# Performance work log

Hardware: AMD Instinct MI355X
Metric: run time of the kernel (lower is better)

The kernel has to match this reference:

```python
import jax, jax.numpy as jnp
from jax import lax
import numpy as np

B, NR, NC, FEAT = 8, 1024, 1024, 768
N = NR + NC
HID, GATD, GRUD = 256, 128, 64
NEG = -9e15  # matches -9000000000000000.0 in torch source


def setup_inputs() -> dict:
    key = jax.random.key(0)
    ks = jax.random.split(key, 24)
    s = 0.02
    nrm = lambda k, shp: jax.random.normal(k, shp, jnp.float32) * s
    z = lambda shp: jnp.zeros(shp, jnp.float32)
    inp = {}
    inp['req_nodes'] = jax.random.normal(ks[0], (B, NR, FEAT), jnp.float32)
    inp['code_nodes'] = jax.random.normal(ks[1], (B, NC, FEAT), jnp.float32)
    inp['alignment_matrix'] = jax.random.bernoulli(ks[2], 0.05, (B, N, N)).astype(jnp.float32)
    inp['total_nodes'] = jax.random.randint(ks[3], (B,), N // 2, N + 1).astype(jnp.int32)
    # feature_projection
    inp['W_proj'] = nrm(ks[4], (HID, FEAT)); inp['b_proj'] = z((HID,))
    # GAT layer 1 (HID->HID), attention weight a is Linear(2*HID, 1, bias=False)
    inp['W_g1'] = nrm(ks[5], (HID, HID)); inp['b_g1'] = z((HID,)); inp['a_g1'] = nrm(ks[6], (2 * HID,))
    # GAT layer 2 (HID->GATD)
    inp['W_g2'] = nrm(ks[7], (GATD, HID)); inp['b_g2'] = z((GATD,)); inp['a_g2'] = nrm(ks[8], (2 * GATD,))
    # bidirectional GRU (torch layout: [3H, in], gates r|z|n)
    inp['Wih_f'] = nrm(ks[9], (3 * GRUD, GATD)); inp['Whh_f'] = nrm(ks[10], (3 * GRUD, GRUD))
    inp['bih_f'] = z((3 * GRUD,)); inp['bhh_f'] = z((3 * GRUD,))
    inp['Wih_b'] = nrm(ks[11], (3 * GRUD, GATD)); inp['Whh_b'] = nrm(ks[12], (3 * GRUD, GRUD))
    inp['bih_b'] = z((3 * GRUD,)); inp['bhh_b'] = z((3 * GRUD,))
    inp['W_fus'] = nrm(ks[13], (GRUD, 2 * GRUD)); inp['b_fus'] = z((GRUD,))
    inp['W_c1'] = nrm(ks[14], (HID // 2, GRUD)); inp['b_c1'] = z((HID // 2,))
    inp['W_c2'] = nrm(ks[15], (1, HID // 2)); inp['b_c2'] = z((1,))
    return inp


def _gat_layer(x, adj, mask, W, b, a):
    # h: [B, N, D]
    h = x @ W.T + b
    D = h.shape[-1]
    # attention(concat(h_i, h_j)) == a[:D]@h_i + a[D:]@h_j -> never materialize [B,N,N,2D]
    s_src = h @ a[:D]   # [B, N]
    s_dst = h @ a[D:]   # [B, N]
    e = jax.nn.leaky_relu(s_src[:, :, None] + s_dst[:, None, :], 0.01)  # [B,N,N]
    att = jax.nn.softmax(jnp.where(adj > 0, e, NEG), axis=-1)
    out = jnp.einsum('bij,bjd->bid', att, h)
    return out * mask[..., None]


def _gru_dir(xproj, Whh, bhh, reverse):
    # xproj: [B, T, 3H] = x @ Wih.T + bih (precomputed)
    Bv, H = xproj.shape[0], Whh.shape[1]
    def step(h, xt):
        gh = h @ Whh.T + bhh
        ir, iz, inn = jnp.split(xt, 3, axis=-1)
        hr, hz, hn = jnp.split(gh, 3, axis=-1)
        r = jax.nn.sigmoid(ir + hr)
        zt = jax.nn.sigmoid(iz + hz)
        n = jnp.tanh(inn + r * hn)
        hnew = (1.0 - zt) * n + zt * h
        return hnew, hnew
    h0 = jnp.zeros((Bv, H), xproj.dtype)
    _, ys = lax.scan(step, h0, jnp.swapaxes(xproj, 0, 1), reverse=reverse)
    return jnp.swapaxes(ys, 0, 1)  # [B, T, H]


def _forward(req_nodes, code_nodes, alignment_matrix, total_nodes,
             W_proj, b_proj, W_g1, b_g1, a_g1, W_g2, b_g2, a_g2,
             Wih_f, Whh_f, bih_f, bhh_f, Wih_b, Whh_b, bih_b, bhh_b,
             W_fus, b_fus, W_c1, b_c1, W_c2, b_c2):
    x = jnp.concatenate([req_nodes, code_nodes], axis=1)        # [B, N, FEAT]
    proj = jax.nn.relu(x @ W_proj.T + b_proj)                   # dropout is eval-mode identity
    Nt = proj.shape[1]
    mask = (jnp.arange(Nt)[None, :] < total_nodes[:, None]).astype(proj.dtype)  # [B, N]
    g1 = _gat_layer(proj, alignment_matrix, mask, W_g1, b_g1, a_g1)
    g1 = jax.nn.relu(g1) * mask[..., None]
    gat_out = _gat_layer(g1, alignment_matrix, mask, W_g2, b_g2, a_g2)
    gat_out = gat_out * mask[..., None]  # extra masking as in torch source (idempotent)
    gf = _gru_dir(gat_out @ Wih_f.T + bih_f, Whh_f, bhh_f, reverse=False)
    gb = _gru_dir(gat_out @ Wih_b.T + bih_b, Whh_b, bhh_b, reverse=True)
    gru_out = jnp.concatenate([gf, gb], axis=-1) * mask[..., None]  # [B, N, 2*GRUD]
    fused = gru_out @ W_fus.T + b_fus                               # [B, N, GRUD]
    pooled = jnp.mean(fused, axis=1)  # AdaptiveAvgPool1d(1) over seq dim
    h1 = jax.nn.relu(pooled @ W_c1.T + b_c1)
    out = jax.nn.sigmoid(h1 @ W_c2.T + b_c2)  # [B, 1]
    return out


def reference(req_nodes, code_nodes, alignment_matrix, total_nodes,
              W_proj, b_proj, W_g1, b_g1, a_g1, W_g2, b_g2, a_g2,
              Wih_f, Whh_f, bih_f, bhh_f, Wih_b, Whh_b, bih_b, bhh_b,
              W_fus, b_fus, W_c1, b_c1, W_c2, b_c2):
    return _forward(req_nodes, code_nodes, alignment_matrix, total_nodes,
                    W_proj, b_proj, W_g1, b_g1, a_g1, W_g2, b_g2, a_g2,
                    Wih_f, Whh_f, bih_f, bhh_f, Wih_b, Whh_b, bih_b, bhh_b,
                    W_fus, b_fus, W_c1, b_c1, W_c2, b_c2)
```

## Files before the change

### kernel.cpp

```cpp
#include <hip/hip_runtime.h>
#include <stdint.h>

#define EMAX 256

typedef short bf16x8 __attribute__((ext_vector_type(8)));
typedef float f32x4 __attribute__((ext_vector_type(4)));
typedef _Float16 h2_t __attribute__((ext_vector_type(2)));

#define SWZ(r, c) ((r) * 64 + ((c) ^ (((r) & 7) << 3)))
#define SWZ256(r, c) ((r) * 256 + ((c) ^ (((r) & 7) << 3)))

__device__ __forceinline__ uint16_t f2bf(float f) {
    union { float f; uint32_t u; } v; v.f = f;
    uint32_t u = v.u;
    uint32_t r = (u + 0x7FFFu + ((u >> 16) & 1u)) >> 16;
    return (uint16_t)r;
}
__device__ __forceinline__ float bf2f(uint16_t h) {
    union { uint32_t u; float f; } v; v.u = ((uint32_t)h) << 16;
    return v.f;
}
__device__ __forceinline__ h2_t u2h2(uint32_t u) {
    union { uint32_t u; h2_t h; } v; v.u = u;
    return v.h;
}
__device__ __forceinline__ uint32_t cvtpk_bf16(float lo, float hi) {
    uint32_t d;
    asm("v_cvt_pk_bf16_f32 %0, %1, %2" : "=v"(d) : "v"(lo), "v"(hi));
    return d;
}

__global__ __launch_bounds__(256) void k_prep(const float* wp, const float* wg1, const float* wg2,
                                              const float* wif, const float* wib,
                                              const float* whf, const float* whb,
                                              const float* bihf, const float* bihb,
                                              uint16_t* op, uint16_t* og1, uint16_t* og2,
                                              uint16_t* oifb, _Float16* ohf, _Float16* ohb, float* bihfb,
                                              float* __restrict__ Sz) {
    int i = blockIdx.x * 256 + threadIdx.x;
    if (i < 196608) op[i]  = f2bf(wp[i]);
    if (i < 65536)  og1[i] = f2bf(wg1[i]);
    if (i < 32768)  og2[i] = f2bf(wg2[i]);
    if (i < 24576)  { oifb[i] = f2bf(wif[i]); oifb[24576 + i] = f2bf(wib[i]); }
    if (i < 12288)  { ohf[i] = (_Float16)whf[i]; ohb[i] = (_Float16)whb[i]; }
    if (i < 192)    { bihfb[i] = bihf[i]; bihfb[192 + i] = bihb[i]; }
    if (i < 1024)   Sz[i] = 0.f;
}

__global__ __launch_bounds__(256) void k_edge(const float* __restrict__ adj,
                                              uint16_t* __restrict__ eidx, int* __restrict__ ecnt) {
    int wid  = threadIdx.x >> 6, lane = threadIdx.x & 63;
    int gw   = blockIdx.x * 4 + wid;
    const float4* base = (const float4*)adj + lane;
    float4 va[8], vb[8];
#define LOADROW(dst, r) { const float4* p_ = base + (size_t)(r) * 512; \
        _Pragma("unroll") for (int c_ = 0; c_ < 8; ++c_) dst[c_] = p_[c_ * 64]; }
#define PROCROW(src, r) { \
        uint32_t m4[8]; int c4[8]; \
        _Pragma("unroll") for (int c_ = 0; c_ < 8; ++c_) { \
            uint32_t m_ = (src[c_].x > 0.f ? 1u : 0u) | (src[c_].y > 0.f ? 2u : 0u) \
                        | (src[c_].z > 0.f ? 4u : 0u) | (src[c_].w > 0.f ? 8u : 0u); \
            m4[c_] = m_; c4[c_] = __popc(m_); } \
        int pk[4]; \
        _Pragma("unroll") for (int q_ = 0; q_ < 4; ++q_) pk[q_] = c4[2*q_] | (c4[2*q_+1] << 16); \
        _Pragma("unroll") for (int off_ = 1; off_ < 64; off_ <<= 1) { \
            _Pragma("unroll") for (int q_ = 0; q_ < 4; ++q_) { \
                int o_ = __shfl_up(pk[q_], off_); \
                if (lane >= off_) pk[q_] += o_; } } \
        uint16_t* outr = eidx + (size_t)(r) * EMAX; \
        int bse = 0; \
        _Pragma("unroll") for (int c_ = 0; c_ < 8; ++c_) { \
            int incl = (pk[c_ >> 1] >> ((c_ & 1) * 16)) & 0xffff; \
            int Tc_  = __shfl(incl, 63); \
            int p_   = bse + incl - c4[c_]; \
            uint32_t mm = m4[c_]; \
            int cb = c_ * 256 + lane * 4; \
            while (mm) { int k_ = __builtin_ctz(mm); mm &= mm - 1u; \
                if (p_ < EMAX) outr[p_] = (uint16_t)(cb + k_); ++p_; } \
            bse += Tc_; } \
        if (lane == 0) ecnt[r] = (bse < EMAX) ? bse : EMAX; }

    LOADROW(va, gw)
#pragma unroll
    for (int it = 0; it < 4; ++it) {
        int rA = gw + (2 * it) * 2048;
        int rB = rA + 2048;
        LOADROW(vb, rB)
        PROCROW(va, rA)
        if (it < 3) LOADROW(va, rB + 2048)
        PROCROW(vb, rB)
    }
#undef LOADROW
#undef PROCROW
}

__global__ __launch_bounds__(256) void k_l1(const float* __restrict__ req, const float* __restrict__ code,
                                            const uint16_t* __restrict__ Wp, const float* __restrict__ bp,
                                            const uint16_t* __restrict__ Wg1, const float* __restrict__ bg1,
                                            const float* __restrict__ a1,
                                            uint16_t* __restrict__ H1,
                                            float* __restrict__ s1src, float* __restrict__ s1dst) {
    __shared__ __align__(16) uint16_t As[64 * 64];
    __shared__ __align__(16) uint16_t Bs[4][64 * 64];
    __shared__ __align__(16) uint16_t Ps[64 * 256];
    int tid = threadIdx.x;
    int m0 = blockIdx.x * 64;
    int wave = tid >> 6, lane = tid & 63;
    int quad = lane >> 4, l16 = lane & 15;
    int ar = tid >> 3, ac = (tid & 7) * 8;
    f32x4 acc[16] = {};
    const float4* rowp[2];
#pragma unroll
    for (int h = 0; h < 2; ++h) {
        int n = m0 + ar + h * 32;
        int b = n >> 11, n2 = n & 2047;
        const float* s = (n2 < 1024) ? (req  + ((size_t)(b * 1024 + n2)) * 768)
                                     : (code + ((size_t)(b * 1024 + (n2 - 1024))) * 768);
        rowp[h] = (const float4*)s + (ac >> 2);
    }
    for (int kb = 0; kb < 768; kb += 64) {
#pragma unroll
        for (int h = 0; h < 2; ++h) {
            float4 f0 = rowp[h][(kb >> 2) + 0];
            float4 f1 = rowp[h][(kb >> 2) + 1];
            uint4 pk;
            pk.x = cvtpk_bf16(f0.x, f0.y); pk.y = cvtpk_bf16(f0.z, f0.w);
            pk.z = cvtpk_bf16(f1.x, f1.y); pk.w = cvtpk_bf16(f1.z, f1.w);
            *(uint4*)&As[SWZ(ar + h * 32, ac)] = pk;
        }
#pragma unroll
        for (int h = 0; h < 8; ++h) {
            int grow = ar + h * 32;
            *(uint4*)&Bs[grow >> 6][SWZ(grow & 63, ac)] =
                *(const uint4*)(Wp + (size_t)grow * 768 + kb + ac);
        }
        __syncthreads();
#pragma unroll
        for (int kk = 0; kk < 64; kk += 32) {
            bf16x8 af = *(bf16x8*)&As[SWZ(wave * 16 + l16, kk + quad * 8)];
#pragma unroll
            for (int c = 0; c < 16; ++c) {
                bf16x8 bfr = *(bf16x8*)&Bs[c >> 2][SWZ((c & 3) * 16 + l16, kk + quad * 8)];
                acc[c] = __builtin_amdgcn_mfma_f32_16x16x32_bf16(af, bfr, acc[c], 0, 0, 0);
            }
        }
        __syncthreads();
    }
#pragma unroll
    for (int c = 0; c < 16; ++c) {
        int col = c * 16 + l16;
        float bv = bp[col];
#pragma unroll
        for (int rg = 0; rg < 4; ++rg) {
            int row = wave * 16 + quad * 4 + rg;
            float v = fmaxf(acc[c][rg] + bv, 0.f);
            Ps[row * 256 + (col ^ ((row & 7) << 3))] = f2bf(v);
            acc[c][rg] = 0.f;
        }
    }
    __syncthreads();
    for (int kb = 0; kb < 256; kb += 64) {
#pragma unroll
        for (int h = 0; h < 8; ++h) {
            int grow = ar + h * 32;
            *(uint4*)&Bs[grow >> 6][SWZ(grow & 63, ac)] =
                *(const uint4*)(Wg1 + (size_t)grow * 256 + kb + ac);
        }
        __syncthreads();
#pragma unroll
        for (int kk = 0; kk < 64; kk += 32) {
            int row = wave * 16 + l16;
            int kcol = kb + kk + quad * 8;
            bf16x8 af = *(bf16x8*)&Ps[row * 256 + (kcol ^ ((row & 7) << 3))];
#pragma unroll
            for (int c = 0; c < 16; ++c) {
                bf16x8 bfr = *(bf16x8*)&Bs[c >> 2][SWZ((c & 3) * 16 + l16, kk + quad * 8)];
                acc[c] = __builtin_amdgcn_mfma_f32_16x16x32_bf16(af, bfr, acc[c], 0, 0, 0);
            }
        }
        __syncthreads();
    }
    float sA[4] = {0.f, 0.f, 0.f, 0.f}, sB[4] = {0.f, 0.f, 0.f, 0.f};
#pragma unroll
    for (int c = 0; c < 16; ++c) {
        int col = c * 16 + l16;
        float bv = bg1[col];
        float av1 = a1[col], av2 = a1[256 + col];
#pragma unroll
        for (int rg = 0; rg < 4; ++rg) {
            int row = m0 + wave * 16 + quad * 4 + rg;
            uint16_t hb = f2bf(acc[c][rg] + bv);
            H1[(size_t)row * 256 + col] = hb;
            float vr = bf2f(hb);
            sA[rg] = fmaf(vr, av1, sA[rg]);
            sB[rg] = fmaf(vr, av2, sB[rg]);
        }
    }
#pragma unroll
    for (int off = 1; off < 16; off <<= 1) {
#pragma unroll
        for (int rg = 0; rg < 4; ++rg) {
            sA[rg] += __shfl_xor(sA[rg], off);
            sB[rg] += __shfl_xor(sB[rg], off);
        }
    }
    if (l16 == 0) {
#pragma unroll
        for (int rg = 0; rg < 4; ++rg) {
            int row = m0 + wave * 16 + quad * 4 + rg;
            s1src[row] = sA[rg];
            s1dst[row] = sB[rg];
        }
    }
}

__global__ __launch_bounds__(256) void k_l2(const uint16_t* __restrict__ G1,
                                            const uint16_t* __restrict__ Wg2,
                                            const float* __restrict__ bg2,
                                            const float* __restrict__ a2,
                                            uint16_t* __restrict__ H2,
                                            float* __restrict__ s2src, float* __restrict__ s2dst) {
    __shared__ __align__(16) uint16_t As[64 * 64];
    __shared__ __align__(16) uint16_t Bs[2][64 * 64];
    int tid = threadIdx.x;
    int m0 = blockIdx.x * 64;
    int wave = tid >> 6, lane = tid & 63;
    int quad = lane >> 4, l16 = lane & 15;
    int ar = tid >> 3, ac = (tid & 7) * 8;
    f32x4 acc[8] = {};
    for (int kb = 0; kb < 256; kb += 64) {
        *(uint4*)&As[SWZ(ar, ac)]      = *(const uint4*)(G1 + (size_t)(m0 + ar)      * 256 + kb + ac);
        *(uint4*)&As[SWZ(ar + 32, ac)] = *(const uint4*)(G1 + (size_t)(m0 + ar + 32) * 256 + kb + ac);
#pragma unroll
        for (int h = 0; h < 4; ++h) {
            int grow = ar + h * 32;
            *(uint4*)&Bs[grow >> 6][SWZ(grow & 63, ac)] =
                *(const uint4*)(Wg2 + (size_t)grow * 256 + kb + ac);
        }
        __syncthreads();
#pragma unroll
        for (int kk = 0; kk < 64; kk += 32) {
            bf16x8 af = *(bf16x8*)&As[SWZ(wave * 16 + l16, kk + quad * 8)];
#pragma unroll
            for (int c = 0; c < 8; ++c) {
                bf16x8 bfr = *(bf16x8*)&Bs[c >> 2][SWZ((c & 3) * 16 + l16, kk + quad * 8)];
                acc[c] = __builtin_amdgcn_mfma_f32_16x16x32_bf16(af, bfr, acc[c], 0, 0, 0);
            }
        }
        __syncthreads();
    }
    float sA[4] = {0.f, 0.f, 0.f, 0.f}, sB[4] = {0.f, 0.f, 0.f, 0.f};
#pragma unroll
    for (int c = 0; c < 8; ++c) {
        int col = c * 16 + l16;
        float bv = bg2[col];
        float av1 = a2[col], av2 = a2[128 + col];
#pragma unroll
        for (int rg = 0; rg < 4; ++rg) {
            int row = m0 + wave * 16 + quad * 4 + rg;
            uint16_t hb = f2bf(acc[c][rg] + bv);
            H2[(size_t)row * 128 + col] = hb;
            float vr = bf2f(hb);
            sA[rg] = fmaf(vr, av1, sA[rg]);
            sB[rg] = fmaf(vr, av2, sB[rg]);
        }
    }
#pragma unroll
    for (int off = 1; off < 16; off <<= 1) {
#pragma unroll
        for (int rg = 0; rg < 4; ++rg) {
            sA[rg] += __shfl_xor(sA[rg], off);
            sB[rg] += __shfl_xor(sB[rg], off);
        }
    }
    if (l16 == 0) {
#pragma unroll
        for (int rg = 0; rg < 4; ++rg) {
            int row = m0 + wave * 16 + quad * 4 + rg;
            s2src[row] = sA[rg];
            s2dst[row] = sB[rg];
        }
    }
}

template<int ACT, int MODE>
__global__ __launch_bounds__(256) void k_gemm(const uint16_t* __restrict__ A,
                                              const uint16_t* __restrict__ Bw,
                                              const float* __restrict__ bias,
                                              void* __restrict__ Cv, void* __restrict__ Cv2,
                                              int M, int N, int K) {
    __shared__ __align__(16) uint16_t As[64 * 64];
    __shared__ __align__(16) uint16_t Bs[64 * 64];
    int tid = threadIdx.x;
    int n0 = blockIdx.x * 64, m0 = blockIdx.y * 64;
    int wave = tid >> 6, lane = tid & 63;
    int quad = lane >> 4, l16 = lane & 15;
    f32x4 acc[4] = {};
    int ar = tid >> 3;
    int ac = (tid & 7) * 8;
    for (int kb = 0; kb < K; kb += 64) {
        *(uint4*)&As[SWZ(ar, ac)]      = *(const uint4*)(A  + (size_t)(m0 + ar)      * K + kb + ac);
        *(uint4*)&As[SWZ(ar + 32, ac)] = *(const uint4*)(A  + (size_t)(m0 + ar + 32) * K + kb + ac);
        *(uint4*)&Bs[SWZ(ar, ac)]      = *(const uint4*)(Bw + (size_t)(n0 + ar)      * K + kb + ac);
        *(uint4*)&Bs[SWZ(ar + 32, ac)] = *(const uint4*)(Bw + (size_t)(n0 + ar + 32) * K + kb + ac);
        __syncthreads();
#pragma unroll
        for (int kk = 0; kk < 64; kk += 32) {
            bf16x8 af = *(bf16x8*)&As[SWZ(wave * 16 + l16, kk + quad * 8)];
#pragma unroll
            for (int c = 0; c < 4; ++c) {
                bf16x8 bfr = *(bf16x8*)&Bs[SWZ(c * 16 + l16, kk + quad * 8)];
                acc[c] = __builtin_amdgcn_mfma_f32_16x16x32_bf16(af, bfr, acc[c], 0, 0, 0);
            }
        }
        __syncthreads();
    }
#pragma unroll
    for (int c = 0; c < 4; ++c) {
        int col = n0 + c * 16 + l16;
        float bv = bias ? bias[col] : 0.f;
#pragma unroll
        for (int rg = 0; rg < 4; ++rg) {
            int row = m0 + wave * 16 + quad * 4 + rg;
            float v = acc[c][rg] + bv;
            if (ACT == 1) v = fmaxf(v, 0.f);
            if (MODE == 1)      ((uint16_t*)Cv)[(size_t)row * N + col] = f2bf(v);
            else if (MODE == 0) ((float*)Cv)[(size_t)row * N + col] = v;
            else {
                int tc = (col < 192) ? col : col - 192;
                int dc = (tc & 63) * 4 + (tc >> 6);
                float* dst = (col < 192) ? (float*)Cv : (float*)Cv2;
                dst[(size_t)row * 256 + dc] = v;
            }
        }
    }
}

#define ACC4(hv, wv) { \
    a0 = fmaf(wv, bf2f((uint16_t)(hv).x), a0); \
    a1 = fmaf(wv, bf2f((uint16_t)((hv).x >> 16)), a1); \
    a2 = fmaf(wv, bf2f((uint16_t)(hv).y), a2); \
    a3 = fmaf(wv, bf2f((uint16_t)((hv).y >> 16)), a3); }

template<int D, int LAYER1>
__global__ __launch_bounds__(256) void k_agg(const uint16_t* __restrict__ H,
                                             const float* __restrict__ ssrc,
                                             const float* __restrict__ sdst,
                                             const uint16_t* __restrict__ eidx,
                                             const int* __restrict__ ecnt,
                                             const int* __restrict__ total,
                                             uint16_t* __restrict__ out) {
    constexpr int LPG = (D == 256) ? 64 : 32;
    constexpr int G   = 64 / LPG;
    constexpr int RS  = D / 4;
    __shared__ __align__(16) uint2 ew[4][EMAX];
    int tid  = threadIdx.x;
    int wid  = tid >> 6, lane = tid & 63;
    int grp  = lane / LPG;
    int c    = lane % LPG;
    int b    = blockIdx.x & 7;
    int i    = ((blockIdx.x >> 3) << 2) + wid;
    int row  = (b << 11) + i;
    uint2* orow = (uint2*)(out + (size_t)row * D);
    if (i >= total[b]) {
        if (grp == 0) { uint2 z; z.x = 0u; z.y = 0u; orow[c] = z; }
        return;
    }
    int cnt = ecnt[row];
    const uint2* H2 = (const uint2*)(H + (size_t)b * 2048 * D);
    float a0 = 0.f, a1 = 0.f, a2 = 0.f, a3 = 0.f;
    if (cnt > 0) {
        float sv = ssrc[row];
        const uint16_t* er = eidx + (size_t)row * EMAX;
        int   jj[4]; float ee[4];
#pragma unroll
        for (int k = 0; k < 4; ++k) {
            int t = lane + 64 * k;
            int j = (t < cnt) ? (int)er[t] : 0;
            float x = sv + sdst[b * 2048 + j];
            float e = (x > 0.f) ? x : 0.01f * x;
            if (t >= cnt) e = -1e30f;
            jj[k] = j; ee[k] = e;
        }
        float m = fmaxf(fmaxf(ee[0], ee[1]), fmaxf(ee[2], ee[3]));
#pragma unroll
        for (int off = 32; off; off >>= 1) m = fmaxf(m, __shfl_xor(m, off));
        float w[4]; float s = 0.f;
#pragma unroll
        for (int k = 0; k < 4; ++k) { w[k] = __expf(ee[k] - m); s += w[k]; }
#pragma unroll
        for (int off = 32; off; off >>= 1) s += __shfl_xor(s, off);
        float inv = 1.f / s;
#pragma unroll
        for (int k = 0; k < 4; ++k) {
            uint2 p; p.x = (uint32_t)jj[k]; p.y = __float_as_uint(w[k] * inv);
            ew[wid][lane + 64 * k] = p;
        }
        asm volatile("s_waitcnt lgkmcnt(0)" ::: "memory");
        constexpr int EPB = 4 * G;
        int cntP = (cnt + EPB - 1) & ~(EPB - 1);
        if constexpr (G == 1) {
            for (int t = 0; t < cntP; t += 4) {
                uint2 e0 = ew[wid][t + 0], e1 = ew[wid][t + 1];
                uint2 e2 = ew[wid][t + 2], e3 = ew[wid][t + 3];
                uint2 h0 = H2[(size_t)e0.x * RS + c];
                uint2 h1 = H2[(size_t)e1.x * RS + c];
                uint2 h2 = H2[(size_t)e2.x * RS + c];
                uint2 h3 = H2[(size_t)e3.x * RS + c];
                ACC4(h0, __uint_as_float(e0.y));
                ACC4(h1, __uint_as_float(e1.y));
                ACC4(h2, __uint_as_float(e2.y));
                ACC4(h3, __uint_as_float(e3.y));
            }
        } else {
            for (int t = 0; t < cntP; t += 8) {
                uint2 e0 = ew[wid][t + 0 + grp], e1 = ew[wid][t + 2 + grp];
                uint2 e2 = ew[wid][t + 4 + grp], e3 = ew[wid][t + 6 + grp];
                uint2 h0 = H2[(size_t)e0.x * RS + c];
                uint2 h1 = H2[(size_t)e1.x * RS + c];
                uint2 h2 = H2[(size_t)e2.x * RS + c];
                uint2 h3 = H2[(size_t)e3.x * RS + c];
                ACC4(h0, __uint_as_float(e0.y));
                ACC4(h1, __uint_as_float(e1.y));
                ACC4(h2, __uint_as_float(e2.y));
                ACC4(h3, __uint_as_float(e3.y));
            }
        }
    } else {
        for (int t = grp; t < 2048; t += G) {
            uint2 hv = H2[(size_t)t * RS + c];
            ACC4(hv, 1.f);
        }
        a0 *= (1.f / 2048.f); a1 *= (1.f / 2048.f);
        a2 *= (1.f / 2048.f); a3 *= (1.f / 2048.f);
    }
    if constexpr (G == 2) {
        a0 += __shfl_xor(a0, 32); a1 += __shfl_xor(a1, 32);
        a2 += __shfl_xor(a2, 32); a3 += __shfl_xor(a3, 32);
    }
    if (LAYER1) {
        a0 = fmaxf(a0, 0.f); a1 = fmaxf(a1, 0.f);
        a2 = fmaxf(a2, 0.f); a3 = fmaxf(a3, 0.f);
    }
    if (grp == 0) {
        uint2 pk;
        pk.x = (uint32_t)f2bf(a0) | ((uint32_t)f2bf(a1) << 16);
        pk.y = (uint32_t)f2bf(a2) | ((uint32_t)f2bf(a3) << 16);
        orow[c] = pk;
    }
}

#define CHUNKS 16
#define CLEN   128
#define WARM   64
#define FDOT2(acc, p, wq) acc = __builtin_amdgcn_fdot2(p, u2h2(wq), acc, false)
#define DOTBLK(hq, q) { \
    h2_t p0 = u2h2(hq.x), p1 = u2h2(hq.y), p2 = u2h2(hq.z), p3 = u2h2(hq.w); \
    FDOT2(ar0, p0, wr[4*q+0]); FDOT2(ar1, p1, wr[4*q+1]); FDOT2(ar2, p2, wr[4*q+2]); FDOT2(ar3, p3, wr[4*q+3]); \
    FDOT2(az0, p0, wz[4*q+0]); FDOT2(az1, p1, wz[4*q+1]); FDOT2(az2, p2, wz[4*q+2]); FDOT2(az3, p3, wz[4*q+3]); \
    FDOT2(an0, p0, wn[4*q+0]); FDOT2(an1, p1, wn[4*q+1]); FDOT2(an2, p2, wn[4*q+2]); FDOT2(an3, p3, wn[4*q+3]); }
#define GRU_STEP(xq) { \
    uint4 h0 = hv4[0], h1 = hv4[1], h2v = hv4[2], h3 = hv4[3]; \
    uint4 h4 = hv4[4], h5 = hv4[5], h6 = hv4[6], h7 = hv4[7]; \
    float ar0 = br, ar1 = 0.f, ar2 = 0.f, ar3 = 0.f; \
    float az0 = bz, az1 = 0.f, az2 = 0.f, az3 = 0.f; \
    float an0 = bn, an1 = 0.f, an2 = 0.f, an3 = 0.f; \
    DOTBLK(h0, 0) DOTBLK(h1, 1) DOTBLK(h2v, 2) DOTBLK(h3, 3) \
    DOTBLK(h4, 4) DOTBLK(h5, 5) DOTBLK(h6, 6) DOTBLK(h7, 7) \
    float ghr = (ar0 + ar1) + (ar2 + ar3); \
    float ghz = (az0 + az1) + (az2 + az3); \
    float ghn = (an0 + an1) + (an2 + an3); \
    float er = __expf(-(xq.x + ghr)); \
    float r = __builtin_amdgcn_rcpf(1.f + er); \
    float ez = __expf(-(xq.y + ghz)); \
    float z = __builtin_amdgcn_rcpf(1.f + ez); \
    float nv = fmaf(r, ghn, xq.z); \
    float en = __expf(-2.f * nv); \
    float n = fmaf(-2.f, __builtin_amdgcn_rcpf(1.f + en), 1.f); \
    hj = fmaf(z, hj - n, n); \
    sj += (t < Tcur) ? hj : 0.f; \
    hb[j] = (_Float16)hj; \
    asm volatile("" ::: "memory"); \
    t += dt; }

__global__ __attribute__((amdgpu_flat_work_group_size(64, 64), amdgpu_waves_per_eu(1, 1)))
void k_gru(const float* __restrict__ XPf, const float* __restrict__ XPb,
           const _Float16* __restrict__ WhF, const _Float16* __restrict__ WhB,
           const float* __restrict__ bhh_f, const float* __restrict__ bhh_b,
           const int* __restrict__ total,
           float* __restrict__ S) {
    int blk   = blockIdx.x;
    int chunk = blk & (CHUNKS - 1);
    int sc    = blk >> 4;
    int dir   = sc >> 3;
    int b     = sc & 7;
    int j     = threadIdx.x;
    const float* XP  = dir ? XPb : XPf;
    const uint32_t* Wd = (const uint32_t*)(dir ? WhB : WhF);
    const float* bhh = dir ? bhh_b : bhh_f;
    uint32_t wr[32], wz[32], wn[32];
#pragma unroll
    for (int c = 0; c < 32; ++c) {
        wr[c] = Wd[(size_t)(      j) * 32 + c];
        wz[c] = Wd[(size_t)( 64 + j) * 32 + c];
        wn[c] = Wd[(size_t)(128 + j) * 32 + c];
    }
    float br = bhh[j], bz = bhh[64 + j], bn = bhh[128 + j];
    __shared__ __align__(16) _Float16 hbuf[64];
    _Float16* hb = hbuf;
    hb[j] = (_Float16)0.f;
    asm volatile("s_waitcnt lgkmcnt(0)" ::: "memory");
    float hj = 0.f, sj = 0.f;
    int Tb = total[b];
    int s0 = chunk * CLEN - WARM;
    int W0 = WARM;
    if (s0 < 0) { s0 = 0; W0 = 0; }
    const float4* xbase = (const float4*)(XP + (size_t)b * 2048 * 256) + j;
    int xstep = dir ? -64 : 64;
    const float4* xptr = xbase + (size_t)(dir ? (2047 - s0) : s0) * 64;
    float4 x0 = *xptr; xptr += xstep;
    float4 x1 = *xptr; xptr += xstep;
    float4 x2 = *xptr; xptr += xstep;
    float4 x3 = *xptr; xptr += xstep;
    int t = dir ? (2047 - s0) : s0, dt = dir ? -1 : 1;
    const uint4* hv4 = (const uint4*)hb;
    int Tcur = -1;
    for (int su = 0; su < W0; su += 4) {
        GRU_STEP(x0) x0 = *xptr; xptr += xstep;
        GRU_STEP(x1) x1 = *xptr; xptr += xstep;
        GRU_STEP(x2) x2 = *xptr; xptr += xstep;
        GRU_STEP(x3) x3 = *xptr; xptr += xstep;
    }
    Tcur = Tb;
    for (int su = 0; su < CLEN; su += 4) {
        GRU_STEP(x0) x0 = *xptr; xptr += xstep;
        GRU_STEP(x1) x1 = *xptr; xptr += xstep;
        GRU_STEP(x2) x2 = *xptr; xptr += xstep;
        GRU_STEP(x3) x3 = *xptr; xptr += xstep;
    }
    atomicAdd(&S[b * 128 + dir * 64 + j], sj);
}

__global__ __launch_bounds__(128) void k_final(const float* __restrict__ S,
                                               const float* __restrict__ Wfus, const float* __restrict__ bfus,
                                               const float* __restrict__ Wc1, const float* __restrict__ bc1,
                                               const float* __restrict__ Wc2, const float* __restrict__ bc2,
                                               float* __restrict__ out) {
    __shared__ float pool[64];
    __shared__ float red[128];
    int tid = threadIdx.x;
    for (int b = 0; b < 8; ++b) {
        if (tid < 64) {
            float a = 0.f;
            for (int jj = 0; jj < 128; ++jj) a += S[b * 128 + jj] * Wfus[tid * 128 + jj];
            pool[tid] = bfus[tid] + a * (1.f / 2048.f);
        }
        __syncthreads();
        float a1 = 0.f;
        for (int d = 0; d < 64; ++d) a1 += pool[d] * Wc1[tid * 64 + d];
        float h = fmaxf(a1 + bc1[tid], 0.f);
        red[tid] = h * Wc2[tid];
        __syncthreads();
        for (int s = 64; s; s >>= 1) { if (tid < s) red[tid] += red[tid + s]; __syncthreads(); }
        if (tid == 0) out[b] = 1.f / (1.f + __expf(-(red[0] + bc2[0])));
        __syncthreads();
    }
}

extern "C" void kernel_launch(void* const* d_in, const int* in_sizes, int n_in,
                              void* d_out, int out_size, void* d_ws, size_t ws_size,
                              hipStream_t stream) {
    (void)in_sizes; (void)n_in; (void)out_size; (void)ws_size;
    const float* req   = (const float*)d_in[0];
    const float* code  = (const float*)d_in[1];
    const float* adj   = (const float*)d_in[2];
    const int*   total = (const int*)  d_in[3];
    const float* W_proj = (const float*)d_in[4];
    const float* b_proj = (const float*)d_in[5];
    const float* W_g1   = (const float*)d_in[6];
    const float* b_g1   = (const float*)d_in[7];
    const float* a_g1   = (const float*)d_in[8];
    const float* W_g2   = (const float*)d_in[9];
    const float* b_g2   = (const float*)d_in[10];
    const float* a_g2   = (const float*)d_in[11];
    const float* Wih_f  = (const float*)d_in[12];
    const float* Whh_f  = (const float*)d_in[13];
    const float* bih_f  = (const float*)d_in[14];
    const float* bhh_f  = (const float*)d_in[15];
    const float* Wih_b  = (const float*)d_in[16];
    const float* Whh_b  = (const float*)d_in[17];
    const float* bih_b  = (const float*)d_in[18];
    const float* bhh_b  = (const float*)d_in[19];
    const float* W_fus  = (const float*)d_in[20];
    const float* b_fus  = (const float*)d_in[21];
    const float* W_c1   = (const float*)d_in[22];
    const float* b_c1   = (const float*)d_in[23];
    const float* W_c2   = (const float*)d_in[24];
    const float* b_c2   = (const float*)d_in[25];

    char* ws = (char*)d_ws;
    float*    XPf  = (float*)(ws + 4096);
    float*    XPb  = (float*)(ws + 4096 + 16777216 + 4096);
    uint16_t* EIDX = (uint16_t*)(ws + 25169920);
    uint16_t* WPb  = (uint16_t*)(ws + 33570816);
    uint16_t* WG1b = (uint16_t*)(ws + 33964032);
    uint16_t* WG2b = (uint16_t*)(ws + 34095104);
    uint16_t* WIFB = (uint16_t*)(ws + 34160640);
    uint16_t* H1bf = (uint16_t*)(ws + 42650624);
    uint16_t* H2bf = (uint16_t*)(ws + 42650624);
    uint16_t* G2bf = (uint16_t*)(ws + 46844928);
    uint16_t* G1bf = (uint16_t*)(ws + 51039232);
    int*      ECNT = (int*)     (ws + 59427840);
    float* s1src = (float*)(ws + 59493376);
    float* s1dst = (float*)(ws + 59558912);
    float* s2src = (float*)(ws + 59624448);
    float* s2dst = (float*)(ws + 59689984);
    float* Sbuf  = (float*)(ws + 59755520);
    _Float16* WhFh = (_Float16*)(ws + 59759616);
    _Float16* WhBh = (_Float16*)(ws + 59784192);
    float* BIHFB   = (float*)(ws + 59808768);

    k_prep<<<768, 256, 0, stream>>>(W_proj, W_g1, W_g2, Wih_f, Wih_b, Whh_f, Whh_b, bih_f, bih_b,
                                    WPb, WG1b, WG2b, WIFB, WhFh, WhBh, BIHFB, Sbuf);

    k_edge<<<512, 256, 0, stream>>>(adj, EIDX, ECNT);

    k_l1<<<256, 256, 0, stream>>>(req, code, WPb, b_proj, WG1b, b_g1, a_g1, H1bf, s1src, s1dst);
    k_agg<256, 1><<<4096, 256, 0, stream>>>(H1bf, s1src, s1dst, EIDX, ECNT, total, G1bf);

    k_l2<<<256, 256, 0, stream>>>(G1bf, WG2b, b_g2, a_g2, H2bf, s2src, s2dst);
    k_agg<128, 0><<<4096, 256, 0, stream>>>(H2bf, s2src, s2dst, EIDX, ECNT, total, G2bf);

    k_gemm<0, 2><<<dim3(6, 256), 256, 0, stream>>>(G2bf, WIFB, BIHFB, XPf, XPb, 16384, 384, 128);

    k_gru<<<256, 64, 0, stream>>>(XPf, XPb, WhFh, WhBh, bhh_f, bhh_b, total, Sbuf);

    k_final<<<1, 128, 0, stream>>>(Sbuf, W_fus, b_fus, W_c1, b_c1, W_c2, b_c2, (float*)d_out);
}
```

Baseline: 523.0 us.

## Fuse adjacency edge extraction into layer-1 GAT aggregation kernel

Removes the standalone edge-list kernel. The layer-1 aggregation now reads each adjacency row directly, builds a per-lane bitmask, and computes the softmax max and the edge-list prefix scan inside the wave. It writes edge weights to shared memory and also stores eidx/ecnt for layer 2. Normalization by the softmax sum moves to after accumulation. Rows beyond the valid node count now skip reading adjacency at all, which saves a launch and some bandwidth, at the cost of a heavier, more serial prologue in the aggregation kernel.

```diff
diff --git a/kernel.cpp b/kernel.cpp
--- a/kernel.cpp
+++ b/kernel.cpp
@@ -8,7 +8,6 @@
 typedef _Float16 h2_t __attribute__((ext_vector_type(2)));
 
 #define SWZ(r, c) ((r) * 64 + ((c) ^ (((r) & 7) << 3)))
-#define SWZ256(r, c) ((r) * 256 + ((c) ^ (((r) & 7) << 3)))
 
 __device__ __forceinline__ uint16_t f2bf(float f) {
     union { float f; uint32_t u; } v; v.f = f;
@@ -45,53 +44,6 @@
     if (i < 12288)  { ohf[i] = (_Float16)whf[i]; ohb[i] = (_Float16)whb[i]; }
     if (i < 192)    { bihfb[i] = bihf[i]; bihfb[192 + i] = bihb[i]; }
     if (i < 1024)   Sz[i] = 0.f;
-}
-
-__global__ __launch_bounds__(256) void k_edge(const float* __restrict__ adj,
-                                              uint16_t* __restrict__ eidx, int* __restrict__ ecnt) {
-    int wid  = threadIdx.x >> 6, lane = threadIdx.x & 63;
-    int gw   = blockIdx.x * 4 + wid;
-    const float4* base = (const float4*)adj + lane;
-    float4 va[8], vb[8];
-#define LOADROW(dst, r) { const float4* p_ = base + (size_t)(r) * 512; \
-        _Pragma("unroll") for (int c_ = 0; c_ < 8; ++c_) dst[c_] = p_[c_ * 64]; }
-#define PROCROW(src, r) { \
-        uint32_t m4[8]; int c4[8]; \
-        _Pragma("unroll") for (int c_ = 0; c_ < 8; ++c_) { \
-            uint32_t m_ = (src[c_].x > 0.f ? 1u : 0u) | (src[c_].y > 0.f ? 2u : 0u) \
-                        | (src[c_].z > 0.f ? 4u : 0u) | (src[c_].w > 0.f ? 8u : 0u); \
-            m4[c_] = m_; c4[c_] = __popc(m_); } \
-        int pk[4]; \
-        _Pragma("unroll") for (int q_ = 0; q_ < 4; ++q_) pk[q_] = c4[2*q_] | (c4[2*q_+1] << 16); \
-        _Pragma("unroll") for (int off_ = 1; off_ < 64; off_ <<= 1) { \
-            _Pragma("unroll") for (int q_ = 0; q_ < 4; ++q_) { \
-                int o_ = __shfl_up(pk[q_], off_); \
-                if (lane >= off_) pk[q_] += o_; } } \
-        uint16_t* outr = eidx + (size_t)(r) * EMAX; \
-        int bse = 0; \
-        _Pragma("unroll") for (int c_ = 0; c_ < 8; ++c_) { \
-            int incl = (pk[c_ >> 1] >> ((c_ & 1) * 16)) & 0xffff; \
-            int Tc_  = __shfl(incl, 63); \
-            int p_   = bse + incl - c4[c_]; \
-            uint32_t mm = m4[c_]; \
-            int cb = c_ * 256 + lane * 4; \
-            while (mm) { int k_ = __builtin_ctz(mm); mm &= mm - 1u; \
-                if (p_ < EMAX) outr[p_] = (uint16_t)(cb + k_); ++p_; } \
-            bse += Tc_; } \
-        if (lane == 0) ecnt[r] = (bse < EMAX) ? bse : EMAX; }
-
-    LOADROW(va, gw)
-#pragma unroll
-    for (int it = 0; it < 4; ++it) {
-        int rA = gw + (2 * it) * 2048;
-        int rB = rA + 2048;
-        LOADROW(vb, rB)
-        PROCROW(va, rA)
-        if (it < 3) LOADROW(va, rB + 2048)
-        PROCROW(vb, rB)
-    }
-#undef LOADROW
-#undef PROCROW
 }
 
 __global__ __launch_bounds__(256) void k_l1(const float* __restrict__ req, const float* __restrict__ code,
@@ -346,8 +298,9 @@
 __global__ __launch_bounds__(256) void k_agg(const uint16_t* __restrict__ H,
                                              const float* __restrict__ ssrc,
                                              const float* __restrict__ sdst,
-                                             const uint16_t* __restrict__ eidx,
-                                             const int* __restrict__ ecnt,
+                                             const float* __restrict__ adj,
+                                             uint16_t* __restrict__ eidx,
+                                             int* __restrict__ ecnt,
                                              const int* __restrict__ total,
                                              uint16_t* __restrict__ out) {
     constexpr int LPG = (D == 256) ? 64 : 32;
@@ -366,37 +319,112 @@
         if (grp == 0) { uint2 z; z.x = 0u; z.y = 0u; orow[c] = z; }
         return;
     }
-    int cnt = ecnt[row];
     const uint2* H2 = (const uint2*)(H + (size_t)b * 2048 * D);
     float a0 = 0.f, a1 = 0.f, a2 = 0.f, a3 = 0.f;
+    int cnt;
+    float inv = 1.f;
+
+    if constexpr (LAYER1) {
+        float sv = ssrc[row];
+        const float* arow = adj + (size_t)row * 2048;
+        const float* sdr  = sdst + b * 2048;
+        uint32_t mask = 0;
+        float m = -1e30f;
+#pragma unroll
+        for (int g = 0; g < 4; ++g) {
+            float av[8], dv[8];
+#pragma unroll
+            for (int q = 0; q < 8; ++q) {
+                int cc = g * 8 + q;
+                av[q] = arow[cc * 64 + lane];
+                dv[q] = sdr[cc * 64 + lane];
+            }
+#pragma unroll
+            for (int q = 0; q < 8; ++q) {
+                int cc = g * 8 + q;
+                if (av[q] > 0.f) {
+                    mask |= 1u << cc;
+                    float x = sv + dv[q];
+                    float e = (x > 0.f) ? x : 0.01f * x;
+                    m = fmaxf(m, e);
+                }
+            }
+        }
+        int cl = __popc(mask);
+#pragma unroll
+        for (int off = 32; off; off >>= 1) m = fmaxf(m, __shfl_xor(m, off));
+        int incl = cl;
+#pragma unroll
+        for (int off = 1; off < 64; off <<= 1) {
+            int o = __shfl_up(incl, off);
+            if (lane >= off) incl += o;
+        }
+        int tot = __shfl(incl, 63);
+        cnt = (tot < EMAX) ? tot : EMAX;
+        if (lane == 0) ecnt[row] = cnt;
+        if (tot > 0) {
+            uint2 z; z.x = 0u; z.y = 0u;
+#pragma unroll
+            for (int k = 0; k < 4; ++k) ew[wid][lane + 64 * k] = z;
+            asm volatile("s_waitcnt lgkmcnt(0)" ::: "memory");
+            int p = incl - cl;
+            float s = 0.f;
+            uint32_t mm = mask;
+            uint16_t* eout = eidx + (size_t)row * EMAX;
+            while (mm) {
+                int cc = __builtin_ctz(mm);
+                mm &= mm - 1u;
+                int j = cc * 64 + lane;
+                float x = sv + sdr[j];
+                float e = (x > 0.f) ? x : 0.01f * x;
+                float w = __expf(e - m);
+                s += w;
+                if (p < EMAX) {
+                    uint2 pp; pp.x = (uint32_t)j; pp.y = __float_as_uint(w);
+                    ew[wid][p] = pp;
+                    eout[p] = (uint16_t)j;
+                }
+                ++p;
+            }
+#pragma unroll
+            for (int off = 32; off; off >>= 1) s += __shfl_xor(s, off);
+            inv = 1.f / s;
+            asm volatile("s_waitcnt lgkmcnt(0)" ::: "memory");
+        }
+    } else {
+        cnt = ecnt[row];
+        if (cnt > 0) {
+            float sv = ssrc[row];
+            const uint16_t* er = eidx + (size_t)row * EMAX;
+            int   jj[4]; float ee[4];
+#pragma unroll
+            for (int k = 0; k < 4; ++k) {
+                int t = lane + 64 * k;
+                int j = (t < cnt) ? (int)er[t] : 0;
+                float x = sv + sdst[b * 2048 + j];
+                float e = (x > 0.f) ? x : 0.01f * x;
+                if (t >= cnt) e = -1e30f;
+                jj[k] = j; ee[k] = e;
+            }
+            float m = fmaxf(fmaxf(ee[0], ee[1]), fmaxf(ee[2], ee[3]));
+#pragma unroll
+            for (int off = 32; off; off >>= 1) m = fmaxf(m, __shfl_xor(m, off));
+            float w[4]; float s = 0.f;
+#pragma unroll
+            for (int k = 0; k < 4; ++k) { w[k] = __expf(ee[k] - m); s += w[k]; }
+#pragma unroll
+            for (int off = 32; off; off >>= 1) s += __shfl_xor(s, off);
+            float invl = 1.f / s;
+#pragma unroll
+            for (int k = 0; k < 4; ++k) {
+                uint2 p; p.x = (uint32_t)jj[k]; p.y = __float_as_uint(w[k] * invl);
+                ew[wid][lane + 64 * k] = p;
+            }
+            asm volatile("s_waitcnt lgkmcnt(0)" ::: "memory");
+        }
+    }
+
     if (cnt > 0) {
-        float sv = ssrc[row];
-        const uint16_t* er = eidx + (size_t)row * EMAX;
-        int   jj[4]; float ee[4];
-#pragma unroll
-        for (int k = 0; k < 4; ++k) {
-            int t = lane + 64 * k;
-            int j = (t < cnt) ? (int)er[t] : 0;
-            float x = sv + sdst[b * 2048 + j];
-            float e = (x > 0.f) ? x : 0.01f * x;
-            if (t >= cnt) e = -1e30f;
-            jj[k] = j; ee[k] = e;
-        }
-        float m = fmaxf(fmaxf(ee[0], ee[1]), fmaxf(ee[2], ee[3]));
-#pragma unroll
-        for (int off = 32; off; off >>= 1) m = fmaxf(m, __shfl_xor(m, off));
-        float w[4]; float s = 0.f;
-#pragma unroll
-        for (int k = 0; k < 4; ++k) { w[k] = __expf(ee[k] - m); s += w[k]; }
-#pragma unroll
-        for (int off = 32; off; off >>= 1) s += __shfl_xor(s, off);
-        float inv = 1.f / s;
-#pragma unroll
-        for (int k = 0; k < 4; ++k) {
-            uint2 p; p.x = (uint32_t)jj[k]; p.y = __float_as_uint(w[k] * inv);
-            ew[wid][lane + 64 * k] = p;
-        }
-        asm volatile("s_waitcnt lgkmcnt(0)" ::: "memory");
         constexpr int EPB = 4 * G;
         int cntP = (cnt + EPB - 1) & ~(EPB - 1);
         if constexpr (G == 1) {
@@ -426,6 +454,7 @@
                 ACC4(h3, __uint_as_float(e3.y));
             }
         }
+        if constexpr (LAYER1) { a0 *= inv; a1 *= inv; a2 *= inv; a3 *= inv; }
     } else {
         for (int t = grp; t < 2048; t += G) {
             uint2 hv = H2[(size_t)t * RS + c];
@@ -623,13 +652,12 @@
     k_prep<<<768, 256, 0, stream>>>(W_proj, W_g1, W_g2, Wih_f, Wih_b, Whh_f, Whh_b, bih_f, bih_b,
                                     WPb, WG1b, WG2b, WIFB, WhFh, WhBh, BIHFB, Sbuf);
 
-    k_edge<<<512, 256, 0, stream>>>(adj, EIDX, ECNT);
-
     k_l1<<<256, 256, 0, stream>>>(req, code, WPb, b_proj, WG1b, b_g1, a_g1, H1bf, s1src, s1dst);
-    k_agg<256, 1><<<4096, 256, 0, stream>>>(H1bf, s1src, s1dst, EIDX, ECNT, total, G1bf);
+
+    k_agg<256, 1><<<4096, 256, 0, stream>>>(H1bf, s1src, s1dst, adj, EIDX, ECNT, total, G1bf);
 
     k_l2<<<256, 256, 0, stream>>>(G1bf, WG2b, b_g2, a_g2, H2bf, s2src, s2dst);
-    k_agg<128, 0><<<4096, 256, 0, stream>>>(H2bf, s2src, s2dst, EIDX, ECNT, total, G2bf);
+    k_agg<128, 0><<<4096, 256, 0, stream>>>(H2bf, s2src, s2dst, adj, EIDX, ECNT, total, G2bf);
 
     k_gemm<0, 2><<<dim3(6, 256), 256, 0, stream>>>(G2bf, WIFB, BIHFB, XPf, XPb, 16384, 384, 128);
 
```

After: 517.8 us. No clear change (-1.0%).
